# Performance work log

Hardware: AMD Instinct MI355X
Metric: run time of the kernel (lower is better)

Reference implementation:

```python
import jax, jax.numpy as jnp
import numpy as np

IDIM = 128
C = 3
NB_SAMPLES = 128
R = 32768
SH_C0 = 0.28209479177387814
SH_C1 = 0.4886025119029199
SH_C2 = np.array([1.0925484305920792, -1.0925484305920792, 0.31539156525252005,
                  -1.0925484305920792, 0.5462742152960396], dtype=np.float32)


def eval_sh_bases(d):
    # d: (R,3) unit directions -> (R,9) degree-2 real SH basis
    x, y, z = d[:, 0], d[:, 1], d[:, 2]
    return jnp.stack([
        jnp.full_like(x, SH_C0),
        -SH_C1 * y, SH_C1 * z, -SH_C1 * x,
        SH_C2[0] * x * y, SH_C2[1] * y * z,
        SH_C2[2] * (2.0 * z * z - x * x - y * y),
        SH_C2[3] * x * z, SH_C2[4] * (x * x - y * y)], axis=-1)


def trilerp(pts, grid):
    # pts: (N,3) in voxel coords (box_min=0, delta_voxel=1); grid: (D,D,D,F)
    D = grid.shape[0]
    p = jnp.clip(pts, 0.0, D - 1 - 1e-4)
    i0 = jnp.floor(p).astype(jnp.int32)
    w = p - i0.astype(p.dtype)          # (N,3) fractional weights
    i1 = jnp.minimum(i0 + 1, D - 1)
    out = jnp.zeros((pts.shape[0], grid.shape[-1]), dtype=p.dtype)
    for dx in (0, 1):
        wx = w[:, 0] if dx else 1.0 - w[:, 0]
        ix = i1[:, 0] if dx else i0[:, 0]
        for dy in (0, 1):
            wy = w[:, 1] if dy else 1.0 - w[:, 1]
            iy = i1[:, 1] if dy else i0[:, 1]
            for dz in (0, 1):
                wz = w[:, 2] if dz else 1.0 - w[:, 2]
                iz = i1[:, 2] if dz else i0[:, 2]
                out = out + (wx * wy * wz)[:, None] * grid[ix, iy, iz]
    return out


def setup_inputs() -> dict:
    key = jax.random.key(0)
    k = jax.random.split(key, 6)
    x = jax.random.uniform(k[0], (R, 3), jnp.float32) * (IDIM - 1)
    d = jax.random.normal(k[1], (R, 3), jnp.float32)
    d = d / jnp.linalg.norm(d, axis=1, keepdims=True)
    tmin = jax.random.uniform(k[2], (R,), jnp.float32) * 5.0
    tmax = tmin + 20.0 + jax.random.uniform(k[3], (R,), jnp.float32) * 80.0
    grid = jax.random.uniform(k[4], (IDIM, IDIM, IDIM, 9 * C), jnp.float32)
    opacity = jax.random.uniform(k[5], (IDIM, IDIM, IDIM, 1), jnp.float32)
    return {"x": x, "d": d, "tmin": tmin, "tmax": tmax, "grid": grid, "opacity": opacity}


def reference(x, d, tmin, tmax, grid, opacity):
    nb_rays = x.shape[0]
    # samples = arange(0.05, 0.95, 1/nb_samples): S entries
    S = int(np.floor(0.9 * NB_SAMPLES - 1e-6)) + 1
    base = 0.05 + jnp.arange(S, dtype=x.dtype) / NB_SAMPLES            # (S,)
    samples = (tmax - tmin)[:, None] * base[None, :] + tmin[:, None]   # (R,S)
    pts = x[:, None, :] + samples[..., None] * d[:, None, :]           # (R,S,3)
    sh = eval_sh_bases(d)                                              # (R,9)
    flat = pts.reshape(-1, 3)
    coeffs = trilerp(flat, grid).reshape(nb_rays, S, C, 9)             # (R,S,C,9)
    op = jnp.clip(trilerp(flat, opacity), 0.0, 100000.0).reshape(nb_rays, S)
    harm = coeffs * sh[:, None, None, :]                               # (R,S,C,9)
    samples_color = jnp.clip(harm.sum(axis=3) + 0.5, 0.0, 100000.0)    # (R,S,C)
    deltas = samples[:, 1:] - samples[:, :-1]                          # (R,S-1)
    dts = -(deltas * op[:, :-1])
    cum = jnp.concatenate([jnp.zeros((nb_rays, 1), dtype=x.dtype),
                           jnp.cumsum(dts, axis=1)[:, :-1]], axis=1)
    w = jnp.exp(cum) * (1.0 - jnp.exp(dts))                            # (R,S-1)
    rays_color = jnp.sum(w[..., None] * samples_color[:, :-1, :], axis=1)  # (R,C)
    return rays_color
```

## Files before the change

kernel.cpp:

```cpp
#include <hip/hip_runtime.h>

#define NS 115
#define WEPS 5e-5f
#define LOG_TSKIP -6.9078f

typedef float f32x4 __attribute__((ext_vector_type(4)));
typedef float f32x2 __attribute__((ext_vector_type(2)));

struct SH9 { float a,b,c,d,e,f,g,h,i; };

__device__ __forceinline__ f32x4 load4(const float* p) { f32x4 v; __builtin_memcpy(&v, p, 16); return v; }
__device__ __forceinline__ f32x2 load2(const float* p) { f32x2 v; __builtin_memcpy(&v, p, 8);  return v; }

__device__ __forceinline__ void pos_to_cell(float px, float py, float pz,
                                            int& ibase, float* wxs, float* wys, float* wzs) {
    px = fminf(fmaxf(px, 0.0f), 126.9999f);
    py = fminf(fmaxf(py, 0.0f), 126.9999f);
    pz = fminf(fmaxf(pz, 0.0f), 126.9999f);
    int ix = (int)px, iy = (int)py, iz = (int)pz;
    float wx = px - (float)ix, wy = py - (float)iy, wz = pz - (float)iz;
    ibase = (ix << 14) + (iy << 7) + iz;
    wxs[0] = 1.0f - wx; wxs[1] = wx;
    wys[0] = 1.0f - wy; wys[1] = wy;
    wzs[0] = 1.0f - wz; wzs[1] = wz;
}

__device__ __forceinline__ float eval_op(float px, float py, float pz,
                                         const float* __restrict__ opa) {
    int ibase; float wxs[2], wys[2], wzs[2];
    pos_to_cell(px, py, pz, ibase, wxs, wys, wzs);
    float op = 0.0f;
    #pragma unroll
    for (int cx = 0; cx < 2; ++cx)
    #pragma unroll
    for (int cy = 0; cy < 2; ++cy) {
        int idx = ibase + (cx << 14) + (cy << 7);
        f32x2 pr = load2(opa + idx);
        float wxy = wxs[cx] * wys[cy];
        op = fmaf(wxy * wzs[0], pr.x, op);
        op = fmaf(wxy * wzs[1], pr.y, op);
    }
    return fminf(fmaxf(op, 0.0f), 100000.0f);
}

__device__ __forceinline__ float wave_incl_scan(float v, int lane) {
    #pragma unroll
    for (int off = 1; off < 64; off <<= 1) {
        float n = __shfl_up(v, (unsigned)off, 64);
        if (lane >= off) v += n;
    }
    return v;
}

__device__ __forceinline__ SH9 make_sh(float ddx, float ddy, float ddz) {
    SH9 sh;
    sh.a = 0.28209479177387814f;
    sh.b = -0.4886025119029199f * ddy;
    sh.c =  0.4886025119029199f * ddz;
    sh.d = -0.4886025119029199f * ddx;
    sh.e =  1.0925484305920792f * ddx * ddy;
    sh.f = -1.0925484305920792f * ddy * ddz;
    sh.g =  0.31539156525252005f * (2.0f*ddz*ddz - ddx*ddx - ddy*ddy);
    sh.h = -1.0925484305920792f * ddx * ddz;
    sh.i =  0.5462742152960396f * (ddx*ddx - ddy*ddy);
    return sh;
}

__global__ __launch_bounds__(256, 4) void fused_color_kernel(
    const float* __restrict__ x, const float* __restrict__ d,
    const float* __restrict__ tmin, const float* __restrict__ tmax,
    const float* __restrict__ opa, const float* __restrict__ grid,
    float* __restrict__ out, int nrays)
{
    int gtid = blockIdx.x * blockDim.x + threadIdx.x;
    int ray = __builtin_amdgcn_readfirstlane(gtid >> 6);
    int lane = threadIdx.x & 63;
    if (ray >= nrays) return;
    int qd  = lane >> 2;
    int sub = lane & 3;

    float ox = x[3*ray+0], oy = x[3*ray+1], oz = x[3*ray+2];
    float ddx = d[3*ray+0], ddy = d[3*ray+1], ddz = d[3*ray+2];
    float t0 = tmin[ray];
    float range = tmax[ray] - t0;
    float delta = range * 0.0078125f;
    SH9 sh = make_sh(ddx, ddy, ddz);

    float tt = range * (0.05f + (float)lane * 0.0078125f) + t0;
    float px0 = ox + tt*ddx, py0 = oy + tt*ddy, pz0 = oz + tt*ddz;
    float opv = eval_op(px0, py0, pz0, opa);
    float dts = -delta * opv;
    float incl = wave_incl_scan(dts, lane);
    float cum = incl - dts;
    float total0 = __shfl(incl, 63, 64);
    float w0 = __expf(cum) * (1.0f - __expf(dts));

    float w1 = 0.0f;
    if (total0 > LOG_TSKIP) {
        int s1 = 64 + lane;
        float dts1 = 0.0f;
        if (s1 < NS) {
            float t1s = range * (0.05f + (float)s1 * 0.0078125f) + t0;
            float qx = ox + t1s*ddx, qy = oy + t1s*ddy, qz = oz + t1s*ddz;
            dts1 = -delta * eval_op(qx, qy, qz, opa);
        }
        float incl1 = wave_incl_scan(dts1, lane);
        float cum1 = total0 + incl1 - dts1;
        w1 = __expf(cum1) * (1.0f - __expf(dts1));
    }

    float s00,s01,s02,s03,s04,s05,s06,s07;
    float s10,s11,s12,s13,s14,s15,s16,s17;
    if (sub == 0) {
        s00=sh.a;s01=sh.b;s02=sh.c;s03=sh.d;s04=sh.e;s05=sh.f;s06=sh.g;s07=sh.h;
        s10=0.f;s11=0.f;s12=0.f;s13=0.f;s14=0.f;s15=0.f;s16=0.f;s17=0.f;
    } else if (sub == 1) {
        s00=sh.i;s01=0.f;s02=0.f;s03=0.f;s04=0.f;s05=0.f;s06=0.f;s07=0.f;
        s10=0.f;s11=sh.a;s12=sh.b;s13=sh.c;s14=sh.d;s15=sh.e;s16=sh.f;s17=sh.g;
    } else if (sub == 2) {
        s00=sh.h;s01=sh.i;s02=0.f;s03=0.f;s04=0.f;s05=0.f;s06=0.f;s07=0.f;
        s10=0.f;s11=0.f;s12=sh.a;s13=sh.b;s14=sh.c;s15=sh.d;s16=sh.e;s17=sh.f;
    } else {
        s00=0.f;s01=sh.g;s02=sh.h;s03=sh.i;s04=0.f;s05=0.f;s06=0.f;s07=0.f;
        s10=0.f;s11=0.f;s12=0.f;s13=0.f;s14=0.f;s15=0.f;s16=0.f;s17=0.f;
    }
    int offa = (sub == 3) ? 23 : (sub << 3);
    int offb = (sub == 3) ? 23 : offa + 4;

    unsigned long long b0 = __ballot(w0 > WEPS);
    unsigned long long b1 = __ballot(w1 > WEPS);

    float accR = 0.0f, accG = 0.0f, accB = 0.0f;

    #pragma unroll 1
    for (int p = 0; p < 8; ++p) {
        unsigned long long bsel = (p < 4) ? b0 : b1;
        int shl = (p & 3) << 4;
        if (((bsel >> shl) & 0xFFFFull) == 0) continue;
        int s = (p << 4) + qd;
        float ws = __shfl((p < 4) ? w0 : w1, s & 63, 64);
        if (ws > WEPS) {
            float st = range * (0.05f + (float)s * 0.0078125f) + t0;
            float px = ox + st*ddx, py = oy + st*ddy, pz = oz + st*ddz;
            int ibase; float wxs[2], wys[2], wzs[2];
            pos_to_cell(px, py, pz, ibase, wxs, wys, wzs);

            f32x4 va[8], vb[8];
            #pragma unroll
            for (int c = 0; c < 8; ++c) {
                int cx = c >> 2, cy = (c >> 1) & 1, cz = c & 1;
                int idx = ibase + (cx << 14) + (cy << 7) + cz;
                const float* cp = grid + (size_t)idx * 27;
                va[c] = load4(cp + offa);
                vb[c] = load4(cp + offb);
            }

            float d0a = 0.0f, d1a = 0.0f;
            #pragma unroll
            for (int c = 0; c < 8; ++c) {
                int cx = c >> 2, cy = (c >> 1) & 1, cz = c & 1;
                float wc = wxs[cx] * wys[cy] * wzs[cz];
                float f0=va[c].x, f1=va[c].y, f2=va[c].z, f3=va[c].w;
                float f4=vb[c].x, f5=vb[c].y, f6=vb[c].z, f7=vb[c].w;
                float e0 = s00*f0 + s01*f1 + s02*f2 + s03*f3
                         + s04*f4 + s05*f5 + s06*f6 + s07*f7;
                float e1 = s10*f0 + s11*f1 + s12*f2 + s13*f3
                         + s14*f4 + s15*f5 + s16*f6 + s17*f7;
                d0a = fmaf(wc, e0, d0a);
                d1a = fmaf(wc, e1, d1a);
            }

            float rp = (sub < 2)  ? d0a : 0.0f;
            float gp = (sub == 1) ? d1a : ((sub == 2) ? d0a : 0.0f);
            float bp = (sub == 2) ? d1a : ((sub == 3) ? d0a : 0.0f);
            rp += __shfl_xor(rp, 1, 64); rp += __shfl_xor(rp, 2, 64);
            gp += __shfl_xor(gp, 1, 64); gp += __shfl_xor(gp, 2, 64);
            bp += __shfl_xor(bp, 1, 64); bp += __shfl_xor(bp, 2, 64);
            float cr = fminf(fmaxf(rp + 0.5f, 0.0f), 100000.0f);
            float cg = fminf(fmaxf(gp + 0.5f, 0.0f), 100000.0f);
            float cb = fminf(fmaxf(bp + 0.5f, 0.0f), 100000.0f);
            accR = fmaf(ws, cr, accR);
            accG = fmaf(ws, cg, accG);
            accB = fmaf(ws, cb, accB);
        }
    }

    #pragma unroll
    for (int off = 4; off < 64; off <<= 1) {
        accR += __shfl_xor(accR, off, 64);
        accG += __shfl_xor(accG, off, 64);
        accB += __shfl_xor(accB, off, 64);
    }
    if (lane == 0) {
        out[3*ray+0] = accR;
        out[3*ray+1] = accG;
        out[3*ray+2] = accB;
    }
}

extern "C" void kernel_launch(void* const* d_in, const int* in_sizes, int n_in,
                              void* d_out, int out_size, void* d_ws, size_t ws_size,
                              hipStream_t stream) {
    const float* x    = (const float*)d_in[0];
    const float* d    = (const float*)d_in[1];
    const float* tmin = (const float*)d_in[2];
    const float* tmax = (const float*)d_in[3];
    const float* grid = (const float*)d_in[4];
    const float* opa  = (const float*)d_in[5];
    float* out = (float*)d_out;

    int nrays = in_sizes[0] / 3;
    int blocks = (nrays * 64 + 255) / 256;

    (void)d_ws; (void)ws_size;
    fused_color_kernel<<<blocks, 256, 0, stream>>>(x, d, tmin, tmax, opa, grid, out, nrays);
}
```

Measured before the change: 381.0 us.

## Issue both opacity sample batches up front and use inline-asm batched grid loads

Computes cell positions for both 64-sample opacity halves and issues all eight opacity loads together before a single wait, so the second half's fetch no longer waits behind the first scan. Grid coefficient loads switch to inline-asm global_load_dwordx4 followed by one explicit vmcnt(0) wait and a scheduling barrier, to force all 16 loads in flight at once. In exchange, the second-half opacity loads are always issued even when early termination would skip them, and the inline asm prevents the compiler from scheduling or merging these loads. The load addresses for sample indices beyond NS still stay within the grid because positions are clamped.

```diff
diff --git a/kernel.cpp b/kernel.cpp
--- a/kernel.cpp
+++ b/kernel.cpp
@@ -9,8 +9,20 @@
 
 struct SH9 { float a,b,c,d,e,f,g,h,i; };
 
-__device__ __forceinline__ f32x4 load4(const float* p) { f32x4 v; __builtin_memcpy(&v, p, 16); return v; }
-__device__ __forceinline__ f32x2 load2(const float* p) { f32x2 v; __builtin_memcpy(&v, p, 8);  return v; }
+__device__ __forceinline__ f32x4 aload4(const float* p) {
+    f32x4 v;
+    asm volatile("global_load_dwordx4 %0, %1, off" : "=v"(v) : "v"(p));
+    return v;
+}
+__device__ __forceinline__ f32x2 aload2(const float* p) {
+    f32x2 v;
+    asm volatile("global_load_dwordx2 %0, %1, off" : "=v"(v) : "v"(p));
+    return v;
+}
+__device__ __forceinline__ void vwait0() {
+    asm volatile("s_waitcnt vmcnt(0)" ::: "memory");
+    __builtin_amdgcn_sched_barrier(0);
+}
 
 __device__ __forceinline__ void pos_to_cell(float px, float py, float pz,
                                             int& ibase, float* wxs, float* wys, float* wzs) {
@@ -23,24 +35,6 @@
     wxs[0] = 1.0f - wx; wxs[1] = wx;
     wys[0] = 1.0f - wy; wys[1] = wy;
     wzs[0] = 1.0f - wz; wzs[1] = wz;
-}
-
-__device__ __forceinline__ float eval_op(float px, float py, float pz,
-                                         const float* __restrict__ opa) {
-    int ibase; float wxs[2], wys[2], wzs[2];
-    pos_to_cell(px, py, pz, ibase, wxs, wys, wzs);
-    float op = 0.0f;
-    #pragma unroll
-    for (int cx = 0; cx < 2; ++cx)
-    #pragma unroll
-    for (int cy = 0; cy < 2; ++cy) {
-        int idx = ibase + (cx << 14) + (cy << 7);
-        f32x2 pr = load2(opa + idx);
-        float wxy = wxs[cx] * wys[cy];
-        op = fmaf(wxy * wzs[0], pr.x, op);
-        op = fmaf(wxy * wzs[1], pr.y, op);
-    }
-    return fminf(fmaxf(op, 0.0f), 100000.0f);
 }
 
 __device__ __forceinline__ float wave_incl_scan(float v, int lane) {
@@ -66,6 +60,20 @@
     return sh;
 }
 
+__device__ __forceinline__ float op_from(const f32x2& c00, const f32x2& c01,
+                                         const f32x2& c10, const f32x2& c11,
+                                         const float* wxs, const float* wys,
+                                         const float* wzs) {
+    float op = 0.0f;
+    float w00 = wxs[0]*wys[0], w01 = wxs[0]*wys[1];
+    float w10 = wxs[1]*wys[0], w11 = wxs[1]*wys[1];
+    op = fmaf(w00*wzs[0], c00.x, op); op = fmaf(w00*wzs[1], c00.y, op);
+    op = fmaf(w01*wzs[0], c01.x, op); op = fmaf(w01*wzs[1], c01.y, op);
+    op = fmaf(w10*wzs[0], c10.x, op); op = fmaf(w10*wzs[1], c10.y, op);
+    op = fmaf(w11*wzs[0], c11.x, op); op = fmaf(w11*wzs[1], c11.y, op);
+    return fminf(fmaxf(op, 0.0f), 100000.0f);
+}
+
 __global__ __launch_bounds__(256, 4) void fused_color_kernel(
     const float* __restrict__ x, const float* __restrict__ d,
     const float* __restrict__ tmin, const float* __restrict__ tmax,
@@ -88,8 +96,27 @@
 
     float tt = range * (0.05f + (float)lane * 0.0078125f) + t0;
     float px0 = ox + tt*ddx, py0 = oy + tt*ddy, pz0 = oz + tt*ddz;
-    float opv = eval_op(px0, py0, pz0, opa);
-    float dts = -delta * opv;
+    int ib0; float wxs0[2], wys0[2], wzs0[2];
+    pos_to_cell(px0, py0, pz0, ib0, wxs0, wys0, wzs0);
+
+    int s1 = 64 + lane;
+    float t1s = range * (0.05f + (float)s1 * 0.0078125f) + t0;
+    float qx = ox + t1s*ddx, qy = oy + t1s*ddy, qz = oz + t1s*ddz;
+    int ib1; float wxs1[2], wys1[2], wzs1[2];
+    pos_to_cell(qx, qy, qz, ib1, wxs1, wys1, wzs1);
+
+    f32x2 a00 = aload2(opa + ib0);
+    f32x2 a01 = aload2(opa + ib0 + (1 << 7));
+    f32x2 a10 = aload2(opa + ib0 + (1 << 14));
+    f32x2 a11 = aload2(opa + ib0 + (1 << 14) + (1 << 7));
+    f32x2 b00 = aload2(opa + ib1);
+    f32x2 b01 = aload2(opa + ib1 + (1 << 7));
+    f32x2 b10 = aload2(opa + ib1 + (1 << 14));
+    f32x2 b11 = aload2(opa + ib1 + (1 << 14) + (1 << 7));
+    vwait0();
+
+    float opv0 = op_from(a00, a01, a10, a11, wxs0, wys0, wzs0);
+    float dts = -delta * opv0;
     float incl = wave_incl_scan(dts, lane);
     float cum = incl - dts;
     float total0 = __shfl(incl, 63, 64);
@@ -97,13 +124,8 @@
 
     float w1 = 0.0f;
     if (total0 > LOG_TSKIP) {
-        int s1 = 64 + lane;
-        float dts1 = 0.0f;
-        if (s1 < NS) {
-            float t1s = range * (0.05f + (float)s1 * 0.0078125f) + t0;
-            float qx = ox + t1s*ddx, qy = oy + t1s*ddy, qz = oz + t1s*ddz;
-            dts1 = -delta * eval_op(qx, qy, qz, opa);
-        }
+        float opv1 = op_from(b00, b01, b10, b11, wxs1, wys1, wzs1);
+        float dts1 = (s1 < NS) ? (-delta * opv1) : 0.0f;
         float incl1 = wave_incl_scan(dts1, lane);
         float cum1 = total0 + incl1 - dts1;
         w1 = __expf(cum1) * (1.0f - __expf(dts1));
@@ -127,14 +149,14 @@
     int offa = (sub == 3) ? 23 : (sub << 3);
     int offb = (sub == 3) ? 23 : offa + 4;
 
-    unsigned long long b0 = __ballot(w0 > WEPS);
-    unsigned long long b1 = __ballot(w1 > WEPS);
+    unsigned long long bal0 = __ballot(w0 > WEPS);
+    unsigned long long bal1 = __ballot(w1 > WEPS);
 
     float accR = 0.0f, accG = 0.0f, accB = 0.0f;
 
     #pragma unroll 1
     for (int p = 0; p < 8; ++p) {
-        unsigned long long bsel = (p < 4) ? b0 : b1;
+        unsigned long long bsel = (p < 4) ? bal0 : bal1;
         int shl = (p & 3) << 4;
         if (((bsel >> shl) & 0xFFFFull) == 0) continue;
         int s = (p << 4) + qd;
@@ -151,9 +173,10 @@
                 int cx = c >> 2, cy = (c >> 1) & 1, cz = c & 1;
                 int idx = ibase + (cx << 14) + (cy << 7) + cz;
                 const float* cp = grid + (size_t)idx * 27;
-                va[c] = load4(cp + offa);
-                vb[c] = load4(cp + offb);
+                va[c] = aload4(cp + offa);
+                vb[c] = aload4(cp + offb);
             }
+            vwait0();
 
             float d0a = 0.0f, d1a = 0.0f;
             #pragma unroll
```

Result: no change. 374.5 us (-1.7%).
